# Performance work log

Hardware: AMD Instinct MI355X
Metric: run time of the kernel (lower is better)

## Reference

```python
import jax, jax.numpy as jnp
import numpy as np

E = 29          # number of cell types (TRAINING_CELL_TYPES)
D = 1985        # input gene dim
B = 32768       # batch of cells
ENC = [512, 256, 256]
EPS = 1e-5


def setup_inputs() -> dict:
    key = jax.random.key(0)
    ks = jax.random.split(key, 16)
    inp = {}
    inp["x"] = jax.random.normal(ks[0], (B, D), dtype=jnp.float32)
    inp["labels"] = jax.random.randint(ks[1], (B,), 0, E, dtype=jnp.int32)
    # shared encoder: Linear -> BatchNorm(eval: running stats) -> ReLU, 3 layers
    dims = [D] + ENC
    ki = 2
    for l in range(3):
        fi, fo = dims[l], dims[l + 1]
        inp[f"W{l}"] = jax.random.normal(ks[ki], (fi, fo), jnp.float32) / np.sqrt(fi).astype(np.float32); ki += 1
        inp[f"b{l}"] = jnp.zeros((fo,), jnp.float32)
        inp[f"g{l}"] = jnp.ones((fo,), jnp.float32)    # BN gamma
        inp[f"be{l}"] = jnp.zeros((fo,), jnp.float32)  # BN beta
        inp[f"m{l}"] = jnp.zeros((fo,), jnp.float32)   # BN running mean
        inp[f"v{l}"] = jnp.ones((fo,), jnp.float32)    # BN running var
    # 29 stacked per-cell-type heads: 256 -> 128 -> 64 -> 1 (LayerNorm+ReLU between)
    inp["HW1"] = jax.random.normal(ks[ki], (E, 256, 128), jnp.float32) / 16.0; ki += 1
    inp["Hb1"] = jnp.zeros((E, 128), jnp.float32)
    inp["LG1"] = jnp.ones((E, 128), jnp.float32)
    inp["LB1"] = jnp.zeros((E, 128), jnp.float32)
    inp["HW2"] = jax.random.normal(ks[ki], (E, 128, 64), jnp.float32) / np.sqrt(128).astype(np.float32); ki += 1
    inp["Hb2"] = jnp.zeros((E, 64), jnp.float32)
    inp["LG2"] = jnp.ones((E, 64), jnp.float32)
    inp["LB2"] = jnp.zeros((E, 64), jnp.float32)
    inp["HWo"] = jax.random.normal(ks[ki], (E, 64), jnp.float32) / 8.0; ki += 1
    inp["Hbo"] = jnp.zeros((E,), jnp.float32)
    return inp


def _ln(h, g, b):
    mu = h.mean(-1, keepdims=True)
    var = h.var(-1, keepdims=True)
    return (h - mu) / jnp.sqrt(var + EPS) * g + b


def reference(x, labels,
              W0, b0, g0, be0, m0, v0,
              W1, b1, g1, be1, m1, v1,
              W2, b2, g2, be2, m2, v2,
              HW1, Hb1, LG1, LB1, HW2, Hb2, LG2, LB2, HWo, Hbo):
    # shared encoder (eval-mode BatchNorm, dropout off)
    h = x
    for W, bb, g, be, m, v in ((W0, b0, g0, be0, m0, v0),
                               (W1, b1, g1, be1, m1, v1),
                               (W2, b2, g2, be2, m2, v2)):
        h = h @ W + bb
        h = (h - m) / jnp.sqrt(v + EPS) * g + be
        h = jax.nn.relu(h)
    feats = h  # [B, 256]
    # all-expert dense compute (identical math to per-group routing), then select
    t = jnp.einsum('bd,edh->ebh', feats, HW1) + Hb1[:, None, :]     # [E,B,128]
    t = jax.nn.relu(_ln(t, LG1[:, None, :], LB1[:, None, :]))
    t = jnp.einsum('ebh,ehk->ebk', t, HW2) + Hb2[:, None, :]        # [E,B,64]
    t = jax.nn.relu(_ln(t, LG2[:, None, :], LB2[:, None, :]))
    out_all = jnp.einsum('ebk,ek->eb', t, HWo) + Hbo[:, None]       # [E,B]
    preds = jnp.take_along_axis(out_all, labels[None, :].astype(jnp.int32), axis=0)[0]  # [B]
    return preds
```

## Files before the change

### kernel.cpp

```cpp
#include <hip/hip_runtime.h>
#include <hip/hip_bf16.h>


typedef __bf16 bf16_t;
typedef bf16_t bf16x8 __attribute__((ext_vector_type(8)));
typedef float  f32x4  __attribute__((ext_vector_type(4)));

#define MAX_TILES 544
#define T1_LD 136

__global__ __launch_bounds__(256) void prep_bn_all(
    const float* __restrict__ b0, const float* __restrict__ g0, const float* __restrict__ be0,
    const float* __restrict__ m0, const float* __restrict__ v0,
    const float* __restrict__ b1, const float* __restrict__ g1, const float* __restrict__ be1,
    const float* __restrict__ m1, const float* __restrict__ v1,
    const float* __restrict__ b2i, const float* __restrict__ g2, const float* __restrict__ be2,
    const float* __restrict__ m2, const float* __restrict__ v2,
    float* __restrict__ s0, float* __restrict__ o0,
    float* __restrict__ s1, float* __restrict__ o1,
    float* __restrict__ s2, float* __restrict__ o2) {
    const int bid = blockIdx.x, tid = threadIdx.x;
    const float *b, *g, *be, *m, *v;
    float *s, *o;
    int n;
    if (bid < 2)      { b = b0;  g = g0; be = be0; m = m0; v = v0; s = s0; o = o0; n = bid * 256 + tid; }
    else if (bid == 2){ b = b1;  g = g1; be = be1; m = m1; v = v1; s = s1; o = o1; n = tid; }
    else              { b = b2i; g = g2; be = be2; m = m2; v = v2; s = s2; o = o2; n = tid; }
    float sv = g[n] * rsqrtf(v[n] + 1e-5f);
    s[n] = sv;
    o[n] = (b[n] - m[n]) * sv + be[n];
}

__device__ __forceinline__ void tsp_one(const float* __restrict__ in, bf16_t* __restrict__ out,
                                        const float* __restrict__ scale,
                                        int K, int N, int Kp, unsigned t) {
    const unsigned kchunks = (unsigned)Kp / 8u;
    const unsigned bn = t / kchunks;
    const unsigned kc = t % kchunks;
    const unsigned b  = bn / (unsigned)N;
    const unsigned n  = bn % (unsigned)N;
    const unsigned k0 = kc * 8u;
    const float sc = scale ? scale[n] : 1.f;
    bf16x8 v{};
#pragma unroll
    for (int j = 0; j < 8; ++j) {
        unsigned k = k0 + j;
        v[j] = (k < (unsigned)K) ? (bf16_t)(in[((size_t)b * K + k) * N + n] * sc)
                                 : (bf16_t)0.f;
    }
    *(bf16x8*)&out[((size_t)b * N + n) * Kp + k0] = v;
}

__global__ __launch_bounds__(256) void prep_weights(
    const float* __restrict__ W0, const float* __restrict__ W1, const float* __restrict__ W2,
    const float* __restrict__ HW1, const float* __restrict__ HW2,
    const float* __restrict__ s0, const float* __restrict__ s1, const float* __restrict__ s2,
    bf16_t* __restrict__ Wt0, bf16_t* __restrict__ Wt1, bf16_t* __restrict__ Wt2,
    bf16_t* __restrict__ HW1t, bf16_t* __restrict__ HW2t) {
    unsigned t = blockIdx.x * 256u + threadIdx.x;
    if      (t < 129024u) tsp_one(W0,  Wt0,  s0, 1985, 512, 2016, t);
    else if (t < 145408u) tsp_one(W1,  Wt1,  s1, 512,  256, 512,  t - 129024u);
    else if (t < 153600u) tsp_one(W2,  Wt2,  s2, 256,  256, 256,  t - 145408u);
    else if (t < 272384u) tsp_one(HW1, HW1t, nullptr, 256, 128, 256, t - 153600u);
    else                  tsp_one(HW2, HW2t, nullptr, 128, 64,  128, t - 272384u);
}

template<bool AF32>
__global__ __launch_bounds__(256) void gemm_bias_relu(const void* __restrict__ Av,
                                                      const bf16_t* __restrict__ Bt,
                                                      const float* __restrict__ bias,
                                                      bf16_t* __restrict__ C,
                                                      int M, int N, int K, int KA) {
    __shared__ bf16_t As[128 * 32];
    __shared__ bf16_t Bs[128 * 32];

    const int tid  = threadIdx.x;
    const int bm0  = blockIdx.y * 128;
    const int bn0  = blockIdx.x * 128;
    const int wave = tid >> 6, lane = tid & 63;
    const int wm   = (wave & 1) * 64, wn = (wave >> 1) * 64;
    const int quad = lane >> 4, tq = lane & 15;
    const int xq   = (quad ^ (tq & 3)) << 3;

    f32x4 acc[4][4] = {};

    const int r0 = tid >> 2;
    const int j0 = tid & 3;
    const int c0 = j0 * 8;
    const int sw = ((j0 ^ (r0 & 3)) << 3);

    bf16_t* AsW0 = &As[ r0       * 32 + sw];
    bf16_t* AsW1 = &As[(r0 + 64) * 32 + sw];
    bf16_t* BsW0 = &Bs[ r0       * 32 + sw];
    bf16_t* BsW1 = &Bs[(r0 + 64) * 32 + sw];

    const bf16_t* Ab = (const bf16_t*)Av;
    const float*  Af = (const float*)Av;
    const bf16_t* Bp0 = Bt + (size_t)(bn0 + r0) * K + c0;
    const bf16_t* Bp1 = Bt + (size_t)(bn0 + r0 + 64) * K + c0;

    for (int k0 = 0; k0 < K; k0 += 32) {
        bf16x8 a0, a1;
        if constexpr (AF32) {
            const float* sA0 = Af + (size_t)(bm0 + r0) * KA + k0 + c0;
            const float* sA1 = Af + (size_t)(bm0 + r0 + 64) * KA + k0 + c0;
            if (k0 + 32 <= KA) {
#pragma unroll
                for (int j = 0; j < 8; ++j) { a0[j] = (bf16_t)sA0[j]; a1[j] = (bf16_t)sA1[j]; }
            } else {
#pragma unroll
                for (int j = 0; j < 8; ++j) {
                    bool ok = (k0 + c0 + j) < KA;
                    a0[j] = ok ? (bf16_t)sA0[j] : (bf16_t)0.f;
                    a1[j] = ok ? (bf16_t)sA1[j] : (bf16_t)0.f;
                }
            }
        } else {
            a0 = *(const bf16x8*)(Ab + (size_t)(bm0 + r0) * K + k0 + c0);
            a1 = *(const bf16x8*)(Ab + (size_t)(bm0 + r0 + 64) * K + k0 + c0);
        }
        bf16x8 b0 = *(const bf16x8*)(Bp0 + k0);
        bf16x8 b1 = *(const bf16x8*)(Bp1 + k0);
        __syncthreads();
        *(bf16x8*)AsW0 = a0;
        *(bf16x8*)AsW1 = a1;
        *(bf16x8*)BsW0 = b0;
        *(bf16x8*)BsW1 = b1;
        __syncthreads();

        bf16x8 af[4], bfr[4];
#pragma unroll
        for (int mt = 0; mt < 4; ++mt)
            af[mt] = *(const bf16x8*)&As[(wm + mt * 16 + tq) * 32 + xq];
#pragma unroll
        for (int nt = 0; nt < 4; ++nt)
            bfr[nt] = *(const bf16x8*)&Bs[(wn + nt * 16 + tq) * 32 + xq];
#pragma unroll
        for (int mt = 0; mt < 4; ++mt)
#pragma unroll
            for (int nt = 0; nt < 4; ++nt)
                acc[mt][nt] = __builtin_amdgcn_mfma_f32_16x16x32_bf16(
                    af[mt], bfr[nt], acc[mt][nt], 0, 0, 0);
    }

#pragma unroll
    for (int nt = 0; nt < 4; ++nt) {
        const int col = bn0 + wn + nt * 16 + tq;
        const float bcol = bias[col];
#pragma unroll
        for (int mt = 0; mt < 4; ++mt) {
#pragma unroll
            for (int r = 0; r < 4; ++r) {
                const int row = bm0 + wm + mt * 16 + quad * 4 + r;
                float v = acc[mt][nt][r] + bcol;
                v = v > 0.f ? v : 0.f;
                C[(size_t)row * N + col] = (bf16_t)v;
            }
        }
    }
}

__global__ __launch_bounds__(64) void head_init(int* __restrict__ counts) {
    if (threadIdx.x < 32) counts[threadIdx.x] = 0;
}

__global__ __launch_bounds__(256) void head_hist(const int* __restrict__ labels,
                                                 int* __restrict__ counts) {
    __shared__ int h[32];
    if (threadIdx.x < 32) h[threadIdx.x] = 0;
    __syncthreads();
    int c = blockIdx.x * 256 + threadIdx.x;
    atomicAdd(&h[labels[c]], 1);
    __syncthreads();
    if (threadIdx.x < 32) {
        int v = h[threadIdx.x];
        if (v) atomicAdd(&counts[threadIdx.x], v);
    }
}

__global__ __launch_bounds__(1024) void head_plan(const int* __restrict__ counts,
                                                  int* __restrict__ cursor,
                                                  int4* __restrict__ descs) {
    __shared__ int offs[30];
    __shared__ int toffs[30];
    if (threadIdx.x == 0) {
        int off = 0, toff = 0;
        for (int e = 0; e < 29; ++e) {
            offs[e] = off; toffs[e] = toff;
            int n = counts[e];
            off += n; toff += (n + 63) >> 6;
        }
        offs[29] = off; toffs[29] = toff;
    }
    __syncthreads();
    if (threadIdx.x < 29) cursor[threadIdx.x] = offs[threadIdx.x];
    int t = threadIdx.x;
    if (t < MAX_TILES) {
        int4 d = make_int4(0, 0, 0, 0);
        if (t < toffs[29]) {
            int e = 0;
            while (toffs[e + 1] <= t) ++e;
            int ti = t - toffs[e];
            int n  = counts[e];
            d.x = e;
            d.y = offs[e] + ti * 64;
            d.z = min(64, n - ti * 64);
        }
        descs[t] = d;
    }
}

__global__ __launch_bounds__(256) void head_scatter(const int* __restrict__ labels,
                                                    int* __restrict__ cursor,
                                                    int* __restrict__ perm) {
    int c = blockIdx.x * 256 + threadIdx.x;
    int p = atomicAdd(&cursor[labels[c]], 1);
    perm[p] = c;
}

__global__ __launch_bounds__(256) void head_mfma(const bf16_t* __restrict__ feats,
                                                 const int* __restrict__ perm,
                                                 const int4* __restrict__ descs,
                                                 const bf16_t* __restrict__ HW1t,
                                                 const float* __restrict__ Hb1,
                                                 const float* __restrict__ LG1,
                                                 const float* __restrict__ LB1,
                                                 const bf16_t* __restrict__ HW2t,
                                                 const float* __restrict__ Hb2,
                                                 const float* __restrict__ LG2,
                                                 const float* __restrict__ LB2,
                                                 const float* __restrict__ HWo,
                                                 const float* __restrict__ Hbo,
                                                 float* __restrict__ out) {
    __shared__ bf16_t t1s[64 * T1_LD];

    const int4 d = descs[blockIdx.x];
    const int e = d.x, start = d.y, count = d.z;
    if (count == 0) return;

    const int tid = threadIdx.x, w = tid >> 6, lane = tid & 63;
    const int tq = lane & 15, quad = lane >> 4;
    const int m0 = w * 16;

    const int am = m0 + tq;
    const int ridx = perm[start + ((am < count) ? am : 0)];
    const bf16_t* arow = feats + (size_t)ridx * 256;

    const bf16_t* w1 = HW1t + (size_t)e * 128 * 256;
    f32x4 acc1[8] = {};
#pragma unroll
    for (int ks = 0; ks < 8; ++ks) {
        bf16x8 a = *(const bf16x8*)(arow + ks * 32 + quad * 8);
#pragma unroll
        for (int nt = 0; nt < 8; ++nt) {
            bf16x8 b = *(const bf16x8*)(w1 + (size_t)(nt * 16 + tq) * 256 + ks * 32 + quad * 8);
            acc1[nt] = __builtin_amdgcn_mfma_f32_16x16x32_bf16(a, b, acc1[nt], 0, 0, 0);
        }
    }

    float s1[4] = {}, q1[4] = {};
#pragma unroll
    for (int nt = 0; nt < 8; ++nt) {
        float hb = Hb1[e * 128 + nt * 16 + tq];
#pragma unroll
        for (int r = 0; r < 4; ++r) {
            float v = acc1[nt][r] + hb;
            acc1[nt][r] = v;
            s1[r] += v; q1[r] += v * v;
        }
    }
#pragma unroll
    for (int off = 1; off < 16; off <<= 1)
#pragma unroll
        for (int r = 0; r < 4; ++r) {
            s1[r] += __shfl_xor(s1[r], off);
            q1[r] += __shfl_xor(q1[r], off);
        }
    float mu1[4], rs1[4];
#pragma unroll
    for (int r = 0; r < 4; ++r) {
        mu1[r] = s1[r] * (1.f / 128.f);
        rs1[r] = rsqrtf(q1[r] * (1.f / 128.f) - mu1[r] * mu1[r] + 1e-5f);
    }
#pragma unroll
    for (int nt = 0; nt < 8; ++nt) {
        const int col = nt * 16 + tq;
        const float lg = LG1[e * 128 + col], lb = LB1[e * 128 + col];
#pragma unroll
        for (int r = 0; r < 4; ++r) {
            float t = (acc1[nt][r] - mu1[r]) * rs1[r] * lg + lb;
            t1s[(m0 + quad * 4 + r) * T1_LD + col] = (bf16_t)fmaxf(t, 0.f);
        }
    }
    __syncthreads();

    const bf16_t* w2 = HW2t + (size_t)e * 64 * 128;
    f32x4 acc2[4] = {};
#pragma unroll
    for (int ks = 0; ks < 4; ++ks) {
        bf16x8 a = *(const bf16x8*)&t1s[(m0 + tq) * T1_LD + ks * 32 + quad * 8];
#pragma unroll
        for (int nt = 0; nt < 4; ++nt) {
            bf16x8 b = *(const bf16x8*)(w2 + (size_t)(nt * 16 + tq) * 128 + ks * 32 + quad * 8);
            acc2[nt] = __builtin_amdgcn_mfma_f32_16x16x32_bf16(a, b, acc2[nt], 0, 0, 0);
        }
    }

    float s2[4] = {}, q2[4] = {};
#pragma unroll
    for (int nt = 0; nt < 4; ++nt) {
        float hb = Hb2[e * 64 + nt * 16 + tq];
#pragma unroll
        for (int r = 0; r < 4; ++r) {
            float v = acc2[nt][r] + hb;
            acc2[nt][r] = v;
            s2[r] += v; q2[r] += v * v;
        }
    }
#pragma unroll
    for (int off = 1; off < 16; off <<= 1)
#pragma unroll
        for (int r = 0; r < 4; ++r) {
            s2[r] += __shfl_xor(s2[r], off);
            q2[r] += __shfl_xor(q2[r], off);
        }
    float p[4] = {};
#pragma unroll
    for (int nt = 0; nt < 4; ++nt) {
        const int col = nt * 16 + tq;
        const float lg = LG2[e * 64 + col], lb = LB2[e * 64 + col];
        const float wo = HWo[e * 64 + col];
#pragma unroll
        for (int r = 0; r < 4; ++r) {
            float mu = s2[r] * (1.f / 64.f);
            float rs = rsqrtf(q2[r] * (1.f / 64.f) - mu * mu + 1e-5f);
            float t = (acc2[nt][r] - mu) * rs * lg + lb;
            p[r] += fmaxf(t, 0.f) * wo;
        }
    }
#pragma unroll
    for (int off = 1; off < 16; off <<= 1)
#pragma unroll
        for (int r = 0; r < 4; ++r) p[r] += __shfl_xor(p[r], off);

    if (tq == 0) {
        const float hbo = Hbo[e];
#pragma unroll
        for (int r = 0; r < 4; ++r) {
            int m = m0 + quad * 4 + r;
            if (m < count) out[perm[start + m]] = p[r] + hbo;
        }
    }
}

static const size_t OFF_H0    = 0;
static const size_t OFF_H1    = 33554432;
static const size_t OFF_FEATS = 50331648;
static const size_t OFF_WT0   = 67108864;
static const size_t OFF_WT1   = 69173248;
static const size_t OFF_WT2   = 69435392;
static const size_t OFF_HW1T  = 69566464;
static const size_t OFF_HW2T  = 71467008;
static const size_t OFF_B20   = 71942144;
static const size_t OFF_B21   = 71944192;
static const size_t OFF_B22   = 71945216;
static const size_t OFF_S0    = 71946240;
static const size_t OFF_S1    = 71948288;
static const size_t OFF_S2    = 71949312;
static const size_t OFF_CNT   = 71950336;
static const size_t OFF_CUR   = 71950464;
static const size_t OFF_DESC  = 71950592;
static const size_t OFF_PERM  = 71959296;

extern "C" void kernel_launch(void* const* d_in, const int* in_sizes, int n_in,
                              void* d_out, int out_size, void* d_ws, size_t ws_size,
                              hipStream_t stream) {
    const float* x      = (const float*)d_in[0];
    const int*   labels = (const int*)d_in[1];
    const float* W[3]   = {(const float*)d_in[2], (const float*)d_in[8],  (const float*)d_in[14]};
    const float* bb[3]  = {(const float*)d_in[3], (const float*)d_in[9],  (const float*)d_in[15]};
    const float* g[3]   = {(const float*)d_in[4], (const float*)d_in[10], (const float*)d_in[16]};
    const float* be[3]  = {(const float*)d_in[5], (const float*)d_in[11], (const float*)d_in[17]};
    const float* mm[3]  = {(const float*)d_in[6], (const float*)d_in[12], (const float*)d_in[18]};
    const float* vv[3]  = {(const float*)d_in[7], (const float*)d_in[13], (const float*)d_in[19]};
    const float* HW1 = (const float*)d_in[20];
    const float* Hb1 = (const float*)d_in[21];
    const float* LG1 = (const float*)d_in[22];
    const float* LB1 = (const float*)d_in[23];
    const float* HW2 = (const float*)d_in[24];
    const float* Hb2 = (const float*)d_in[25];
    const float* LG2 = (const float*)d_in[26];
    const float* LB2 = (const float*)d_in[27];
    const float* HWo = (const float*)d_in[28];
    const float* Hbo = (const float*)d_in[29];

    char* ws = (char*)d_ws;
    bf16_t* h0    = (bf16_t*)(ws + OFF_H0);
    bf16_t* h1    = (bf16_t*)(ws + OFF_H1);
    bf16_t* feats = (bf16_t*)(ws + OFF_FEATS);
    bf16_t* Wt0   = (bf16_t*)(ws + OFF_WT0);
    bf16_t* Wt1   = (bf16_t*)(ws + OFF_WT1);
    bf16_t* Wt2   = (bf16_t*)(ws + OFF_WT2);
    bf16_t* HW1t  = (bf16_t*)(ws + OFF_HW1T);
    bf16_t* HW2t  = (bf16_t*)(ws + OFF_HW2T);
    float*  b20   = (float*)(ws + OFF_B20);
    float*  b21   = (float*)(ws + OFF_B21);
    float*  b22   = (float*)(ws + OFF_B22);
    float*  s0    = (float*)(ws + OFF_S0);
    float*  s1    = (float*)(ws + OFF_S1);
    float*  s2    = (float*)(ws + OFF_S2);
    int*    cnt   = (int*)(ws + OFF_CNT);
    int*    cur   = (int*)(ws + OFF_CUR);
    int4*   descs = (int4*)(ws + OFF_DESC);
    int*    perm  = (int*)(ws + OFF_PERM);
    float*  outp  = (float*)d_out;

    prep_bn_all<<<4, 256, 0, stream>>>(bb[0], g[0], be[0], mm[0], vv[0],
                                       bb[1], g[1], be[1], mm[1], vv[1],
                                       bb[2], g[2], be[2], mm[2], vv[2],
                                       s0, b20, s1, b21, s2, b22);
    prep_weights<<<1180, 256, 0, stream>>>(W[0], W[1], W[2], HW1, HW2,
                                           s0, s1, s2, Wt0, Wt1, Wt2, HW1t, HW2t);

    head_init<<<1, 64, 0, stream>>>(cnt);
    head_hist<<<128, 256, 0, stream>>>(labels, cnt);
    head_plan<<<1, 1024, 0, stream>>>(cnt, cur, descs);
    head_scatter<<<128, 256, 0, stream>>>(labels, cur, perm);

    dim3 blk(256);
    dim3 grid0(512 / 128, 32768 / 128);
    gemm_bias_relu<true><<<grid0, blk, 0, stream>>>(x, Wt0, b20, h0, 32768, 512, 2016, 1985);
    dim3 grid1(256 / 128, 32768 / 128);
    gemm_bias_relu<false><<<grid1, blk, 0, stream>>>(h0, Wt1, b21, h1, 32768, 256, 512, 512);
    gemm_bias_relu<false><<<grid1, blk, 0, stream>>>(h1, Wt2, b22, feats, 32768, 256, 256, 256);

    head_mfma<<<MAX_TILES, 256, 0, stream>>>(feats, perm, descs, HW1t, Hb1, LG1, LB1,
                                             HW2t, Hb2, LG2, LB2, HWo, Hbo, outp);
}
```

Baseline: 783.4 us.

## Pre-convert x to padded bf16 and load GEMM tiles directly into LDS

Adds a repack_x pass that turns the fp32 input into a zero-padded bf16 matrix, so the first encoder GEMM shares one bf16 path with the others. The GEMM now moves A and B tiles straight from global memory into LDS with global_load_lds, skipping the register round-trip, and drops the XOR swizzle. It also maps block IDs so groups of 8 row tiles share a column tile, for better cache reuse. The cost is an extra full pass over x with a large scratch buffer, possible LDS bank conflicts without the swizzle, and a rearranged workspace layout where buffers alias.

```diff
diff --git a/kernel.cpp b/kernel.cpp
--- a/kernel.cpp
+++ b/kernel.cpp
@@ -8,6 +8,22 @@
 
 #define MAX_TILES 544
 #define T1_LD 136
+
+__device__ __forceinline__ void gld16(const bf16_t* g, bf16_t* l) {
+    __builtin_amdgcn_global_load_lds(
+        (const __attribute__((address_space(1))) void*)g,
+        (__attribute__((address_space(3))) void*)l,
+        16, 0, 0);
+}
+
+__global__ __launch_bounds__(256) void repack_x(const float* __restrict__ x,
+                                                bf16_t* __restrict__ xp) {
+    const unsigned idx = blockIdx.x * 256u + threadIdx.x;
+    const unsigned r = idx / 2016u;
+    const unsigned c = idx % 2016u;
+    float v = (c < 1985u) ? x[(size_t)r * 1985u + c] : 0.f;
+    xp[idx] = (bf16_t)v;
+}
 
 __global__ __launch_bounds__(256) void prep_bn_all(
     const float* __restrict__ b0, const float* __restrict__ g0, const float* __restrict__ be0,
@@ -65,76 +81,52 @@
     else                  tsp_one(HW2, HW2t, nullptr, 128, 64,  128, t - 272384u);
 }
 
-template<bool AF32>
-__global__ __launch_bounds__(256) void gemm_bias_relu(const void* __restrict__ Av,
+__global__ __launch_bounds__(256) void gemm_bias_relu(const bf16_t* __restrict__ A,
                                                       const bf16_t* __restrict__ Bt,
                                                       const float* __restrict__ bias,
                                                       bf16_t* __restrict__ C,
-                                                      int M, int N, int K, int KA) {
+                                                      int N, int K, int NT) {
     __shared__ bf16_t As[128 * 32];
     __shared__ bf16_t Bs[128 * 32];
 
-    const int tid  = threadIdx.x;
-    const int bm0  = blockIdx.y * 128;
-    const int bn0  = blockIdx.x * 128;
-    const int wave = tid >> 6, lane = tid & 63;
-    const int wm   = (wave & 1) * 64, wn = (wave >> 1) * 64;
-    const int quad = lane >> 4, tq = lane & 15;
-    const int xq   = (quad ^ (tq & 3)) << 3;
+    const unsigned b = blockIdx.x;
+    const unsigned c8 = b & 7u, t = b >> 3;
+    const int bn0 = (int)(t % (unsigned)NT) * 128;
+    const int bm0 = (int)((t / (unsigned)NT) * 8u + c8) * 128;
+
+    const int tid = threadIdx.x;
+    const int wv = tid >> 6, ln = tid & 63;
+    const int quad = ln >> 4, tq = ln & 15;
+    const int wm = (wv & 1) * 64, wn = (wv >> 1) * 64;
+
+    const int sr = ln >> 2;
+    const int sc = (ln & 3) * 8;
+    bf16_t* lA0 = &As[(wv * 16) * 32];
+    bf16_t* lA1 = &As[(64 + wv * 16) * 32];
+    bf16_t* lB0 = &Bs[(wv * 16) * 32];
+    bf16_t* lB1 = &Bs[(64 + wv * 16) * 32];
+    const bf16_t* gA0 = A + (size_t)(bm0 + wv * 16 + sr) * K + sc;
+    const bf16_t* gA1 = A + (size_t)(bm0 + 64 + wv * 16 + sr) * K + sc;
+    const bf16_t* gB0 = Bt + (size_t)(bn0 + wv * 16 + sr) * K + sc;
+    const bf16_t* gB1 = Bt + (size_t)(bn0 + 64 + wv * 16 + sr) * K + sc;
 
     f32x4 acc[4][4] = {};
 
-    const int r0 = tid >> 2;
-    const int j0 = tid & 3;
-    const int c0 = j0 * 8;
-    const int sw = ((j0 ^ (r0 & 3)) << 3);
-
-    bf16_t* AsW0 = &As[ r0       * 32 + sw];
-    bf16_t* AsW1 = &As[(r0 + 64) * 32 + sw];
-    bf16_t* BsW0 = &Bs[ r0       * 32 + sw];
-    bf16_t* BsW1 = &Bs[(r0 + 64) * 32 + sw];
-
-    const bf16_t* Ab = (const bf16_t*)Av;
-    const float*  Af = (const float*)Av;
-    const bf16_t* Bp0 = Bt + (size_t)(bn0 + r0) * K + c0;
-    const bf16_t* Bp1 = Bt + (size_t)(bn0 + r0 + 64) * K + c0;
-
     for (int k0 = 0; k0 < K; k0 += 32) {
-        bf16x8 a0, a1;
-        if constexpr (AF32) {
-            const float* sA0 = Af + (size_t)(bm0 + r0) * KA + k0 + c0;
-            const float* sA1 = Af + (size_t)(bm0 + r0 + 64) * KA + k0 + c0;
-            if (k0 + 32 <= KA) {
-#pragma unroll
-                for (int j = 0; j < 8; ++j) { a0[j] = (bf16_t)sA0[j]; a1[j] = (bf16_t)sA1[j]; }
-            } else {
-#pragma unroll
-                for (int j = 0; j < 8; ++j) {
-                    bool ok = (k0 + c0 + j) < KA;
-                    a0[j] = ok ? (bf16_t)sA0[j] : (bf16_t)0.f;
-                    a1[j] = ok ? (bf16_t)sA1[j] : (bf16_t)0.f;
-                }
-            }
-        } else {
-            a0 = *(const bf16x8*)(Ab + (size_t)(bm0 + r0) * K + k0 + c0);
-            a1 = *(const bf16x8*)(Ab + (size_t)(bm0 + r0 + 64) * K + k0 + c0);
-        }
-        bf16x8 b0 = *(const bf16x8*)(Bp0 + k0);
-        bf16x8 b1 = *(const bf16x8*)(Bp1 + k0);
         __syncthreads();
-        *(bf16x8*)AsW0 = a0;
-        *(bf16x8*)AsW1 = a1;
-        *(bf16x8*)BsW0 = b0;
-        *(bf16x8*)BsW1 = b1;
+        gld16(gA0 + k0, lA0);
+        gld16(gA1 + k0, lA1);
+        gld16(gB0 + k0, lB0);
+        gld16(gB1 + k0, lB1);
         __syncthreads();
 
         bf16x8 af[4], bfr[4];
 #pragma unroll
         for (int mt = 0; mt < 4; ++mt)
-            af[mt] = *(const bf16x8*)&As[(wm + mt * 16 + tq) * 32 + xq];
+            af[mt] = *(const bf16x8*)&As[(wm + mt * 16 + tq) * 32 + quad * 8];
 #pragma unroll
         for (int nt = 0; nt < 4; ++nt)
-            bfr[nt] = *(const bf16x8*)&Bs[(wn + nt * 16 + tq) * 32 + xq];
+            bfr[nt] = *(const bf16x8*)&Bs[(wn + nt * 16 + tq) * 32 + quad * 8];
 #pragma unroll
         for (int mt = 0; mt < 4; ++mt)
 #pragma unroll
@@ -288,8 +280,8 @@
         const float lg = LG1[e * 128 + col], lb = LB1[e * 128 + col];
 #pragma unroll
         for (int r = 0; r < 4; ++r) {
-            float t = (acc1[nt][r] - mu1[r]) * rs1[r] * lg + lb;
-            t1s[(m0 + quad * 4 + r) * T1_LD + col] = (bf16_t)fmaxf(t, 0.f);
+            float tv = (acc1[nt][r] - mu1[r]) * rs1[r] * lg + lb;
+            t1s[(m0 + quad * 4 + r) * T1_LD + col] = (bf16_t)fmaxf(tv, 0.f);
         }
     }
     __syncthreads();
@@ -334,8 +326,8 @@
         for (int r = 0; r < 4; ++r) {
             float mu = s2[r] * (1.f / 64.f);
             float rs = rsqrtf(q2[r] * (1.f / 64.f) - mu * mu + 1e-5f);
-            float t = (acc2[nt][r] - mu) * rs * lg + lb;
-            p[r] += fmaxf(t, 0.f) * wo;
+            float tv = (acc2[nt][r] - mu) * rs * lg + lb;
+            p[r] += fmaxf(tv, 0.f) * wo;
         }
     }
 #pragma unroll
@@ -353,24 +345,25 @@
     }
 }
 
-static const size_t OFF_H0    = 0;
-static const size_t OFF_H1    = 33554432;
-static const size_t OFF_FEATS = 50331648;
-static const size_t OFF_WT0   = 67108864;
-static const size_t OFF_WT1   = 69173248;
-static const size_t OFF_WT2   = 69435392;
-static const size_t OFF_HW1T  = 69566464;
-static const size_t OFF_HW2T  = 71467008;
-static const size_t OFF_B20   = 71942144;
-static const size_t OFF_B21   = 71944192;
-static const size_t OFF_B22   = 71945216;
-static const size_t OFF_S0    = 71946240;
-static const size_t OFF_S1    = 71948288;
-static const size_t OFF_S2    = 71949312;
-static const size_t OFF_CNT   = 71950336;
-static const size_t OFF_CUR   = 71950464;
-static const size_t OFF_DESC  = 71950592;
-static const size_t OFF_PERM  = 71959296;
+static const size_t OFF_XP    = 0;
+static const size_t OFF_H1    = 0;
+static const size_t OFF_FEATS = 16777216;
+static const size_t OFF_H0    = 132120576;
+static const size_t OFF_CNT   = 132120576;
+static const size_t OFF_CUR   = 132120832;
+static const size_t OFF_DESC  = 132121088;
+static const size_t OFF_PERM  = 132136960;
+static const size_t OFF_WT0   = 165675008;
+static const size_t OFF_WT1   = 167739392;
+static const size_t OFF_WT2   = 168001536;
+static const size_t OFF_B20   = 168132608;
+static const size_t OFF_B21   = 168134656;
+static const size_t OFF_B22   = 168135680;
+static const size_t OFF_S0    = 168136704;
+static const size_t OFF_S1    = 168138752;
+static const size_t OFF_S2    = 168139776;
+static const size_t OFF_HW1T  = 168140800;
+static const size_t OFF_HW2T  = 170041344;
 
 extern "C" void kernel_launch(void* const* d_in, const int* in_sizes, int n_in,
                               void* d_out, int out_size, void* d_ws, size_t ws_size,
@@ -395,6 +388,7 @@
     const float* Hbo = (const float*)d_in[29];
 
     char* ws = (char*)d_ws;
+    bf16_t* xp    = (bf16_t*)(ws + OFF_XP);
     bf16_t* h0    = (bf16_t*)(ws + OFF_H0);
     bf16_t* h1    = (bf16_t*)(ws + OFF_H1);
     bf16_t* feats = (bf16_t*)(ws + OFF_FEATS);
@@ -421,18 +415,17 @@
                                        s0, b20, s1, b21, s2, b22);
     prep_weights<<<1180, 256, 0, stream>>>(W[0], W[1], W[2], HW1, HW2,
                                            s0, s1, s2, Wt0, Wt1, Wt2, HW1t, HW2t);
+    repack_x<<<258048, 256, 0, stream>>>(x, xp);
+
+    gemm_bias_relu<<<1024, 256, 0, stream>>>(xp, Wt0, b20, h0, 512, 2016, 4);
+    gemm_bias_relu<<<512,  256, 0, stream>>>(h0, Wt1, b21, h1, 256, 512, 2);
 
     head_init<<<1, 64, 0, stream>>>(cnt);
     head_hist<<<128, 256, 0, stream>>>(labels, cnt);
     head_plan<<<1, 1024, 0, stream>>>(cnt, cur, descs);
     head_scatter<<<128, 256, 0, stream>>>(labels, cur, perm);
 
-    dim3 blk(256);
-    dim3 grid0(512 / 128, 32768 / 128);
-    gemm_bias_relu<true><<<grid0, blk, 0, stream>>>(x, Wt0, b20, h0, 32768, 512, 2016, 1985);
-    dim3 grid1(256 / 128, 32768 / 128);
-    gemm_bias_relu<false><<<grid1, blk, 0, stream>>>(h0, Wt1, b21, h1, 32768, 256, 512, 512);
-    gemm_bias_relu<false><<<grid1, blk, 0, stream>>>(h1, Wt2, b22, feats, 32768, 256, 256, 256);
+    gemm_bias_relu<<<512, 256, 0, stream>>>(h1, Wt2, b22, feats, 256, 256, 2);
 
     head_mfma<<<MAX_TILES, 256, 0, stream>>>(feats, perm, descs, HW1t, Hb1, LG1, LB1,
                                              HW2t, Hb2, LG2, LB2, HWo, Hbo, outp);
```

Measured after the change: 742.2 us. 1.06x faster.
